# Kernel optimization log

Hardware: AMD Instinct MI355X
Metric: run time of the kernel (lower is better)

Reference implementation:

```python
import jax, jax.numpy as jnp
import numpy as np

# Module constants (from init_kwargs)
B, NIN, NOUT = 128, 1024, 1024
G_OFF, G_ON, K_V = 0.001, 0.003, 0.5


def setup_inputs() -> dict:
    key = jax.random.key(0)
    k1, k2, k3 = jax.random.split(key, 3)
    stdv = 1.0 / np.sqrt(NIN)
    x = jax.random.normal(k1, (B, NIN), dtype=jnp.float32)
    # NonNeg-constrained weights, RandomNormal(mean=0.5, std=1/sqrt(in))
    w_pos = jnp.abs(0.5 + stdv * jax.random.normal(k2, (NIN, NOUT), dtype=jnp.float32))
    w_neg = jnp.abs(0.5 + stdv * jax.random.normal(k3, (NIN, NOUT), dtype=jnp.float32))
    b_pos = jnp.full((NOUT,), 0.5, dtype=jnp.float32)
    b_neg = jnp.full((NOUT,), 0.5, dtype=jnp.float32)
    return {"x": x, "w_pos": w_pos, "w_neg": w_neg, "b_pos": b_pos, "b_neg": b_neg}


def reference(x, w_pos, w_neg, b_pos, b_neg):
    # combine_weights(): append bias row, interleave pos/neg columns -> [in+1, 2*out]
    comb_pos = jnp.concatenate([w_pos, b_pos[None, :]], axis=0)  # [in+1, out]
    comb_neg = jnp.concatenate([w_neg, b_neg[None, :]], axis=0)  # [in+1, out]
    weights = jnp.stack([comb_pos, comb_neg], axis=-1).reshape(NIN + 1, 2 * NOUT)

    # append ones column for bias input; scale to voltages
    ones = jnp.ones((x.shape[0], 1), dtype=x.dtype)
    voltages = K_V * jnp.concatenate([x, ones], axis=1)  # [B, in+1]

    # double_weights_to_conductances: linear map of weights into [G_off, G_on]
    max_w = jnp.max(weights)
    k_cond = (G_ON - G_OFF) / max_w
    conductances = k_cond * weights + G_OFF  # [in+1, 2*out]

    # eval path: expand-multiply-reduce == matmul (same math, fused here)
    currents = voltages @ conductances  # [B, 2*out]

    # differential pair readout and rescale back to weight units
    total_currents = currents[:, 0::2] - currents[:, 1::2]  # [B, out]
    y_disturbed = total_currents / (K_V * k_cond)
    return y_disturbed
```

## Files before the change

kernel.cpp:

```cpp
#include <hip/hip_runtime.h>


#define NB   128
#define NIN  1024
#define NOUT 1024

#define OT   32
#define KC   64
#define NKS  (NIN / KC)
#define XP   65

__device__ __forceinline__ unsigned short f32_to_bf16_rne(float f) {
    union { float f; unsigned u; } c; c.f = f;
    unsigned u = c.u + 0x7FFFu + ((c.u >> 16) & 1u);
    return (unsigned short)(u >> 16);
}
__device__ __forceinline__ float bf16_to_f32(unsigned short h) {
    union { unsigned u; float f; } c; c.u = ((unsigned)h) << 16;
    return c.f;
}

__global__ __launch_bounds__(128) void memr_partial(
    const float* __restrict__ x,  const float* __restrict__ wp,
    const float* __restrict__ wn, unsigned short* __restrict__ ws)
{
    __shared__ float xs[NB * XP];
    __shared__ float wd[KC * OT];

    const int t  = threadIdx.x;
    const int o0 = blockIdx.x * OT;
    const int ks = blockIdx.y;
    const int k0 = ks * KC;

    #pragma unroll
    for (int r = 0; r < 16; ++r) {
        const int f4 = r * 128 + t;
        const int b  = f4 >> 4;
        const int q  = f4 & 15;
        const float4 v = *(const float4*)&x[(size_t)b * NIN + k0 + q * 4];
        float* d = &xs[b * XP + q * 4];
        d[0] = v.x; d[1] = v.y; d[2] = v.z; d[3] = v.w;
    }
    #pragma unroll
    for (int r = 0; r < 4; ++r) {
        const int f4 = r * 128 + t;
        const int k  = f4 >> 3;
        const int q  = f4 & 7;
        const size_t g = (size_t)(k0 + k) * NOUT + o0 + q * 4;
        const float4 p = *(const float4*)&wp[g];
        const float4 n = *(const float4*)&wn[g];
        float4 d4;
        d4.x = p.x - n.x; d4.y = p.y - n.y; d4.z = p.z - n.z; d4.w = p.w - n.w;
        *(float4*)&wd[k * OT + q * 4] = d4;
    }
    __syncthreads();

    const int tx = t & 7;
    const int ty = t >> 3;

    float acc[8][4];
    #pragma unroll
    for (int i = 0; i < 8; ++i)
        #pragma unroll
        for (int j = 0; j < 4; ++j) acc[i][j] = 0.f;

    const float* xr = &xs[ty * 8 * XP];
    const float* wr = &wd[tx * 4];

    #pragma unroll 8
    for (int k = 0; k < KC; ++k) {
        const float4 w4 = *(const float4*)&wr[k * OT];
        float xv[8];
        #pragma unroll
        for (int i = 0; i < 8; ++i) xv[i] = xr[i * XP + k];
        #pragma unroll
        for (int i = 0; i < 8; ++i) {
            acc[i][0] += xv[i] * w4.x;
            acc[i][1] += xv[i] * w4.y;
            acc[i][2] += xv[i] * w4.z;
            acc[i][3] += xv[i] * w4.w;
        }
    }

    unsigned short* wsb = ws + (size_t)ks * NB * NOUT;
    #pragma unroll
    for (int i = 0; i < 8; ++i) {
        const int b = ty * 8 + i;
        ushort4 v;
        v.x = f32_to_bf16_rne(acc[i][0]);
        v.y = f32_to_bf16_rne(acc[i][1]);
        v.z = f32_to_bf16_rne(acc[i][2]);
        v.w = f32_to_bf16_rne(acc[i][3]);
        *(ushort4*)&wsb[(size_t)b * NOUT + o0 + tx * 4] = v;
    }
}

__global__ __launch_bounds__(256) void memr_reduce(
    const unsigned short* __restrict__ ws, const float* __restrict__ bp,
    const float* __restrict__ bn, float* __restrict__ out)
{
    const int g  = blockIdx.x * 256 + threadIdx.x;
    const int i8 = g * 8;
    const int o8 = i8 & (NOUT - 1);

    float s[8];
    #pragma unroll
    for (int j = 0; j < 8; ++j) s[j] = bp[o8 + j] - bn[o8 + j];

    #pragma unroll
    for (int ks = 0; ks < NKS; ++ks) {
        const ushort4* p = (const ushort4*)&ws[(size_t)ks * NB * NOUT + i8];
        const ushort4 a = p[0], b4 = p[1];
        const unsigned short u[8] = {a.x, a.y, a.z, a.w, b4.x, b4.y, b4.z, b4.w};
        #pragma unroll
        for (int j = 0; j < 8; ++j)
            s[j] += bf16_to_f32(u[j]);
    }
    float4 lo, hi;
    lo.x = s[0]; lo.y = s[1]; lo.z = s[2]; lo.w = s[3];
    hi.x = s[4]; hi.y = s[5]; hi.z = s[6]; hi.w = s[7];
    *(float4*)&out[i8]     = lo;
    *(float4*)&out[i8 + 4] = hi;
}

extern "C" void kernel_launch(void* const* d_in, const int* in_sizes, int n_in,
                              void* d_out, int out_size, void* d_ws, size_t ws_size,
                              hipStream_t stream)
{
    const float* x  = (const float*)d_in[0];
    const float* wp = (const float*)d_in[1];
    const float* wn = (const float*)d_in[2];
    const float* bp = (const float*)d_in[3];
    const float* bn = (const float*)d_in[4];
    float* out = (float*)d_out;
    unsigned short* ws = (unsigned short*)d_ws;

    dim3 g1(NOUT / OT, NKS);
    memr_partial<<<g1, 128, 0, stream>>>(x, wp, wn, ws);
    memr_reduce<<<NB * NOUT / 8 / 256, 256, 0, stream>>>(ws, bp, bn, out);
}
```

Baseline: 77.40 us.

## Transpose x tile in LDS and use 8x8 register micro-tiles with wider output tile

The output tile widens from 32 to 64 columns and the K chunk shrinks from 64 to 32. x is stored transposed in LDS so each thread can read 8 batch values with float4 loads, and each thread computes an 8x8 register block instead of 8x4, which doubles the FMAs per LDS load. The split-K count doubles, so the bf16 partial workspace and the reduce traffic grow too. The reduce kernel now handles 4 outputs per thread over 32 slices instead of 8 outputs over 16.

```diff
diff --git a/kernel.cpp b/kernel.cpp
--- a/kernel.cpp
+++ b/kernel.cpp
@@ -5,10 +5,11 @@
 #define NIN  1024
 #define NOUT 1024
 
-#define OT   32
-#define KC   64
+#define OT   64
+#define KC   32
 #define NKS  (NIN / KC)
-#define XP   65
+#define XS   132
+#define WDS  68
 
 __device__ __forceinline__ unsigned short f32_to_bf16_rne(float f) {
     union { float f; unsigned u; } c; c.f = f;
@@ -24,8 +25,8 @@
     const float* __restrict__ x,  const float* __restrict__ wp,
     const float* __restrict__ wn, unsigned short* __restrict__ ws)
 {
-    __shared__ float xs[NB * XP];
-    __shared__ float wd[KC * OT];
+    __shared__ float xs[KC * XS];
+    __shared__ float wd[KC * WDS];
 
     const int t  = threadIdx.x;
     const int o0 = blockIdx.x * OT;
@@ -33,65 +34,68 @@
     const int k0 = ks * KC;
 
     #pragma unroll
-    for (int r = 0; r < 16; ++r) {
+    for (int r = 0; r < 8; ++r) {
         const int f4 = r * 128 + t;
-        const int b  = f4 >> 4;
-        const int q  = f4 & 15;
+        const int b  = f4 >> 3;
+        const int q  = f4 & 7;
         const float4 v = *(const float4*)&x[(size_t)b * NIN + k0 + q * 4];
-        float* d = &xs[b * XP + q * 4];
-        d[0] = v.x; d[1] = v.y; d[2] = v.z; d[3] = v.w;
+        xs[(q * 4 + 0) * XS + b] = v.x;
+        xs[(q * 4 + 1) * XS + b] = v.y;
+        xs[(q * 4 + 2) * XS + b] = v.z;
+        xs[(q * 4 + 3) * XS + b] = v.w;
     }
     #pragma unroll
     for (int r = 0; r < 4; ++r) {
         const int f4 = r * 128 + t;
-        const int k  = f4 >> 3;
-        const int q  = f4 & 7;
-        const size_t g = (size_t)(k0 + k) * NOUT + o0 + q * 4;
+        const int kk = f4 >> 4;
+        const int q  = f4 & 15;
+        const size_t g = (size_t)(k0 + kk) * NOUT + o0 + q * 4;
         const float4 p = *(const float4*)&wp[g];
         const float4 n = *(const float4*)&wn[g];
-        float4 d4;
-        d4.x = p.x - n.x; d4.y = p.y - n.y; d4.z = p.z - n.z; d4.w = p.w - n.w;
-        *(float4*)&wd[k * OT + q * 4] = d4;
+        float4 d;
+        d.x = p.x - n.x; d.y = p.y - n.y; d.z = p.z - n.z; d.w = p.w - n.w;
+        *(float4*)&wd[kk * WDS + q * 4] = d;
     }
     __syncthreads();
 
-    const int tx = t & 7;
-    const int ty = t >> 3;
+    const int to = t & 7;
+    const int tb = t >> 3;
 
-    float acc[8][4];
+    float acc[8][8];
     #pragma unroll
     for (int i = 0; i < 8; ++i)
         #pragma unroll
-        for (int j = 0; j < 4; ++j) acc[i][j] = 0.f;
+        for (int j = 0; j < 8; ++j) acc[i][j] = 0.f;
 
-    const float* xr = &xs[ty * 8 * XP];
-    const float* wr = &wd[tx * 4];
+    const float* xr = &xs[tb * 8];
+    const float* wr = &wd[to * 8];
 
-    #pragma unroll 8
-    for (int k = 0; k < KC; ++k) {
-        const float4 w4 = *(const float4*)&wr[k * OT];
-        float xv[8];
+    #pragma unroll 4
+    for (int kk = 0; kk < KC; ++kk) {
+        const float4 xa = *(const float4*)&xr[kk * XS];
+        const float4 xb = *(const float4*)&xr[kk * XS + 4];
+        const float4 wa = *(const float4*)&wr[kk * WDS];
+        const float4 wb = *(const float4*)&wr[kk * WDS + 4];
+        const float xv[8] = {xa.x, xa.y, xa.z, xa.w, xb.x, xb.y, xb.z, xb.w};
+        const float wv[8] = {wa.x, wa.y, wa.z, wa.w, wb.x, wb.y, wb.z, wb.w};
         #pragma unroll
-        for (int i = 0; i < 8; ++i) xv[i] = xr[i * XP + k];
-        #pragma unroll
-        for (int i = 0; i < 8; ++i) {
-            acc[i][0] += xv[i] * w4.x;
-            acc[i][1] += xv[i] * w4.y;
-            acc[i][2] += xv[i] * w4.z;
-            acc[i][3] += xv[i] * w4.w;
-        }
+        for (int i = 0; i < 8; ++i)
+            #pragma unroll
+            for (int j = 0; j < 8; ++j)
+                acc[i][j] += xv[i] * wv[j];
     }
 
-    unsigned short* wsb = ws + (size_t)ks * NB * NOUT;
+    unsigned short* wsb = ws + (size_t)ks * NB * NOUT + o0 + to * 8;
     #pragma unroll
     for (int i = 0; i < 8; ++i) {
-        const int b = ty * 8 + i;
-        ushort4 v;
-        v.x = f32_to_bf16_rne(acc[i][0]);
-        v.y = f32_to_bf16_rne(acc[i][1]);
-        v.z = f32_to_bf16_rne(acc[i][2]);
-        v.w = f32_to_bf16_rne(acc[i][3]);
-        *(ushort4*)&wsb[(size_t)b * NOUT + o0 + tx * 4] = v;
+        const int b = tb * 8 + i;
+        ushort4 v0, v1;
+        v0.x = f32_to_bf16_rne(acc[i][0]); v0.y = f32_to_bf16_rne(acc[i][1]);
+        v0.z = f32_to_bf16_rne(acc[i][2]); v0.w = f32_to_bf16_rne(acc[i][3]);
+        v1.x = f32_to_bf16_rne(acc[i][4]); v1.y = f32_to_bf16_rne(acc[i][5]);
+        v1.z = f32_to_bf16_rne(acc[i][6]); v1.w = f32_to_bf16_rne(acc[i][7]);
+        *(ushort4*)&wsb[(size_t)b * NOUT]     = v0;
+        *(ushort4*)&wsb[(size_t)b * NOUT + 4] = v1;
     }
 }
 
@@ -100,27 +104,22 @@
     const float* __restrict__ bn, float* __restrict__ out)
 {
     const int g  = blockIdx.x * 256 + threadIdx.x;
-    const int i8 = g * 8;
-    const int o8 = i8 & (NOUT - 1);
+    const int i4 = g * 4;
+    const int o4 = i4 & (NOUT - 1);
 
-    float s[8];
-    #pragma unroll
-    for (int j = 0; j < 8; ++j) s[j] = bp[o8 + j] - bn[o8 + j];
+    const float4 bpv = *(const float4*)&bp[o4];
+    const float4 bnv = *(const float4*)&bn[o4];
+    float s0 = bpv.x - bnv.x, s1 = bpv.y - bnv.y;
+    float s2 = bpv.z - bnv.z, s3 = bpv.w - bnv.w;
 
     #pragma unroll
     for (int ks = 0; ks < NKS; ++ks) {
-        const ushort4* p = (const ushort4*)&ws[(size_t)ks * NB * NOUT + i8];
-        const ushort4 a = p[0], b4 = p[1];
-        const unsigned short u[8] = {a.x, a.y, a.z, a.w, b4.x, b4.y, b4.z, b4.w};
-        #pragma unroll
-        for (int j = 0; j < 8; ++j)
-            s[j] += bf16_to_f32(u[j]);
+        const ushort4 u = *(const ushort4*)&ws[(size_t)ks * NB * NOUT + i4];
+        s0 += bf16_to_f32(u.x); s1 += bf16_to_f32(u.y);
+        s2 += bf16_to_f32(u.z); s3 += bf16_to_f32(u.w);
     }
-    float4 lo, hi;
-    lo.x = s[0]; lo.y = s[1]; lo.z = s[2]; lo.w = s[3];
-    hi.x = s[4]; hi.y = s[5]; hi.z = s[6]; hi.w = s[7];
-    *(float4*)&out[i8]     = lo;
-    *(float4*)&out[i8 + 4] = hi;
+    float4 o; o.x = s0; o.y = s1; o.z = s2; o.w = s3;
+    *(float4*)&out[i4] = o;
 }
 
 extern "C" void kernel_launch(void* const* d_in, const int* in_sizes, int n_in,
@@ -137,5 +136,5 @@
 
     dim3 g1(NOUT / OT, NKS);
     memr_partial<<<g1, 128, 0, stream>>>(x, wp, wn, ws);
-    memr_reduce<<<NB * NOUT / 8 / 256, 256, 0, stream>>>(ws, bp, bn, out);
+    memr_reduce<<<NB * NOUT / 4 / 256, 256, 0, stream>>>(ws, bp, bn, out);
 }
```

New measurement: 78.57 us. About the same (+1.5%).
